# Kernel optimization log

Measured on AMD Instinct MI355X. Metric: run time of the kernel, lower is better.

Reference implementation:

```python
import jax, jax.numpy as jnp
import numpy as np

GNO_RADIUS = 0.1
SCALES = (1.0, 2.0)


def _rescale(x):
    # rescale coords per batch/dim to [-1, 1] (matches repo's rescale())
    mn = x.min(axis=1, keepdims=True)
    mx = x.max(axis=1, keepdims=True)
    return 2.0 * (x - mn) / (mx - mn + 1e-12) - 1.0


def setup_inputs() -> dict:
    key = jax.random.key(0)
    ks = jax.random.split(key, 6)
    B, N, M, Din, C, D, H = 2, 1024, 1024, 16, 32, 2, 32
    pndata = jax.random.normal(ks[0], (B, N, Din), dtype=jnp.float32)
    x_coord = jax.random.uniform(ks[1], (B, N, D), dtype=jnp.float32)
    # latent queries: regular 32x32 grid in [-1,1]^2 (regional node positions)
    g = jnp.linspace(-1.0, 1.0, 32, dtype=jnp.float32)
    latent_queries = jnp.stack(jnp.meshgrid(g, g, indexing='ij'), axis=-1).reshape(M, D)
    # lifting ChannelMLP (1 layer == pointwise linear)
    W_lift = jax.random.normal(ks[2], (Din, C), dtype=jnp.float32) / np.sqrt(Din)
    b_lift = jnp.zeros((C,), dtype=jnp.float32)
    # IntegralTransform kernel MLP: [2*D -> H -> C], gelu between layers
    W1 = jax.random.normal(ks[3], (2 * D, H), dtype=jnp.float32) / np.sqrt(2 * D)
    b1 = jnp.zeros((H,), dtype=jnp.float32)
    W2 = jax.random.normal(ks[4], (H, C), dtype=jnp.float32) / np.sqrt(H)
    b2 = jnp.zeros((C,), dtype=jnp.float32)
    return dict(pndata=pndata, x_coord=x_coord, latent_queries=latent_queries,
                W_lift=W_lift, b_lift=b_lift, W1=W1, b1=b1, W2=W2, b2=b2)


def reference(pndata, x_coord, latent_queries, W_lift, b_lift, W1, b1, W2, b2):
    # pndata: [B,N,Din], x_coord: [B,N,D], latent_queries: [M,D]
    x = _rescale(x_coord)                           # [B,N,D]
    f = pndata @ W_lift + b_lift                    # lifting -> [B,N,C]
    q = latent_queries                              # [M,D]
    B, N, D = x.shape
    M = q.shape[0]
    # squared distances query->point: [B,M,N]
    d2 = jnp.sum((q[None, :, None, :] - x[:, None, :, :]) ** 2, axis=-1)
    # kernel MLP input: concat(y_j, x_i) per (query i, point j): [B,M,N,2D]
    feat = jnp.concatenate([
        jnp.broadcast_to(x[:, None, :, :], (B, M, N, D)),
        jnp.broadcast_to(q[None, :, None, :], (B, M, N, D)),
    ], axis=-1)
    k = jax.nn.gelu(feat @ W1 + b1) @ W2 + b2       # [B,M,N,C]
    kv = k * f[:, None, :, :]                       # 'linear' transform: k(x,y) * f(y)
    out = jnp.zeros((B, M, kv.shape[-1]), dtype=kv.dtype)
    for s in SCALES:                                # small fixed scale set
        mask = (d2 <= (GNO_RADIUS * s) ** 2).astype(kv.dtype)   # radius-ball neighbors
        cnt = jnp.maximum(mask.sum(axis=-1), 1.0)               # [B,M]
        agg = jnp.einsum('bmn,bmnc->bmc', mask, kv) / cnt[..., None]  # mean reduce
        out = out + agg                              # sum over scales
    return out
```

## Files before the change

kernel.cpp:

```cpp
#include <hip/hip_runtime.h>

#define BB 2
#define NN 1024
#define MM 1024
#define DIN 16
#define CC 32
#define HH 32

__device__ __forceinline__ float gelu_tanh(float v) {
    float v3 = v * v * v;
    float u = 0.7978845608028654f * (v + 0.044715f * v3);
    float e = __expf(2.0f * u);
    float t = 1.0f - 2.0f / (e + 1.0f);
    return 0.5f * v * (1.0f + t);
}

__global__ __launch_bounds__(256) void gno_fused(
    const float* __restrict__ pndata, const float* __restrict__ x_coord,
    const float* __restrict__ latq,
    const float* __restrict__ W_lift, const float* __restrict__ b_lift,
    const float* __restrict__ W1, const float* __restrict__ b1,
    const float* __restrict__ W2, const float* __restrict__ b2,
    float* __restrict__ out)
{
    const int bid = blockIdx.x;
    const int b = bid >> 10;
    const int i = bid & 1023;
    const int t = threadIdx.x;
    const int lane = t & 63;
    const int wave = t >> 6;
    const int g = t >> 5;
    const int c = t & 31;

    __shared__ float2 nbr_xy[NN];
    __shared__ unsigned nbr_meta[NN];
    __shared__ __align__(16) float hbuf[8 * HH];
    __shared__ float accs[8 * CC];
    __shared__ float redf[4 * 4];
    __shared__ int kcnt[4];
    __shared__ int k1cnt[4];

    const float w1a = W1[c];
    const float w1b = W1[HH + c];
    const float w1c = W1[2 * HH + c];
    const float w1d = W1[3 * HH + c];
    const float b1v = b1[c];
    const float b2v = b2[c];
    const float blv = b_lift[c];
    float wl[DIN];
    #pragma unroll
    for (int k = 0; k < DIN; ++k) wl[k] = W_lift[k * CC + c];
    float w2c[HH];
    #pragma unroll
    for (int h = 0; h < HH; ++h) w2c[h] = W2[h * CC + c];

    const float q0 = latq[2 * i];
    const float q1 = latq[2 * i + 1];

    const float2* xcb = (const float2*)x_coord + b * NN;
    float2 xyc[4];
    float mn0 = 1e30f, mx0 = -1e30f, mn1 = 1e30f, mx1 = -1e30f;
    #pragma unroll
    for (int kk = 0; kk < 4; ++kk) {
        xyc[kk] = xcb[wave * 256 + kk * 64 + lane];
        mn0 = fminf(mn0, xyc[kk].x); mx0 = fmaxf(mx0, xyc[kk].x);
        mn1 = fminf(mn1, xyc[kk].y); mx1 = fmaxf(mx1, xyc[kk].y);
    }
    #pragma unroll
    for (int off = 32; off > 0; off >>= 1) {
        mn0 = fminf(mn0, __shfl_down(mn0, off));
        mx0 = fmaxf(mx0, __shfl_down(mx0, off));
        mn1 = fminf(mn1, __shfl_down(mn1, off));
        mx1 = fmaxf(mx1, __shfl_down(mx1, off));
    }
    if (lane == 0) {
        redf[wave * 4 + 0] = mn0; redf[wave * 4 + 1] = mx0;
        redf[wave * 4 + 2] = mn1; redf[wave * 4 + 3] = mx1;
    }
    __syncthreads();
    const float Amn0 = fminf(fminf(redf[0], redf[4]),  fminf(redf[8],  redf[12]));
    const float Amx0 = fmaxf(fmaxf(redf[1], redf[5]),  fmaxf(redf[9],  redf[13]));
    const float Amn1 = fminf(fminf(redf[2], redf[6]),  fminf(redf[10], redf[14]));
    const float Amx1 = fmaxf(fmaxf(redf[3], redf[7]),  fmaxf(redf[11], redf[15]));
    const float den0 = __fadd_rn(__fsub_rn(Amx0, Amn0), 1e-12f);
    const float den1 = __fadd_rn(__fsub_rn(Amx1, Amn1), 1e-12f);

    const float t1 = 0.01f;
    const float t2 = 0.04f;

    const unsigned long long lmask = (1ull << lane) - 1ull;
    int kw = 0, k1w = 0;
    #pragma unroll
    for (int kk = 0; kk < 4; ++kk) {
        const int j = wave * 256 + kk * 64 + lane;
        float r0 = __fsub_rn(__fdiv_rn(__fmul_rn(2.0f, __fsub_rn(xyc[kk].x, Amn0)), den0), 1.0f);
        float r1 = __fsub_rn(__fdiv_rn(__fmul_rn(2.0f, __fsub_rn(xyc[kk].y, Amn1)), den1), 1.0f);
        float dx = __fsub_rn(q0, r0);
        float dy = __fsub_rn(q1, r1);
        float d2 = __fadd_rn(__fmul_rn(dx, dx), __fmul_rn(dy, dy));
        bool h2 = d2 <= t2;
        bool h1 = d2 <= t1;
        unsigned long long m2 = __ballot(h2);
        unsigned long long m1 = __ballot(h1);
        if (h2) {
            int idx = wave * 256 + kw + __popcll(m2 & lmask);
            nbr_meta[idx] = (unsigned)j | (h1 ? 1024u : 0u);
            nbr_xy[idx] = make_float2(r0, r1);
        }
        kw += (int)__popcll(m2);
        k1w += (int)__popcll(m1);
    }
    if (lane == 0) { kcnt[wave] = kw; k1cnt[wave] = k1w; }
    __syncthreads();

    const int Ks0 = kcnt[0], Ks1 = kcnt[1], Ks2 = kcnt[2], Ks3 = kcnt[3];
    const int K2 = Ks0 + Ks1 + Ks2 + Ks3;
    const int c1 = k1cnt[0] + k1cnt[1] + k1cnt[2] + k1cnt[3];
    const float inv1 = 1.0f / fmaxf((float)c1, 1.0f);
    const float inv2 = 1.0f / fmaxf((float)K2, 1.0f);
    const float ci = fmaf(q1, w1d, fmaf(q0, w1c, b1v));

    float acc = 0.0f;
    #pragma unroll
    for (int seg = 0; seg < 4; ++seg) {
        const int Ks = (seg == 0) ? Ks0 : (seg == 1) ? Ks1 : (seg == 2) ? Ks2 : Ks3;
        const int base = seg * 256;
        const int nt = (Ks + 7) >> 3;
        for (int it = 0; it < nt; ++it) {
            const int ib = it * 8 + g;
            const bool active = ib < Ks;
            const int idx = base + (active ? ib : 0);
            const unsigned meta = nbr_meta[idx];
            const float2 xy = nbr_xy[idx];
            const int j = (int)(meta & 1023u);
            const float w = ((meta & 1024u) ? inv1 : 0.0f) + inv2;

            float pre = fmaf(xy.y, w1b, fmaf(xy.x, w1a, ci));
            hbuf[g * HH + c] = gelu_tanh(pre);

            float kc = b2v;
            const float4* hb4 = (const float4*)&hbuf[g * HH];
            #pragma unroll
            for (int hh = 0; hh < 8; ++hh) {
                float4 hv = hb4[hh];
                kc = fmaf(hv.x, w2c[4 * hh + 0], kc);
                kc = fmaf(hv.y, w2c[4 * hh + 1], kc);
                kc = fmaf(hv.z, w2c[4 * hh + 2], kc);
                kc = fmaf(hv.w, w2c[4 * hh + 3], kc);
            }

            const float4* pd4 = (const float4*)&pndata[(b * NN + j) * DIN];
            float fv = blv;
            #pragma unroll
            for (int k4 = 0; k4 < 4; ++k4) {
                float4 p = pd4[k4];
                fv = fmaf(p.x, wl[4 * k4 + 0], fv);
                fv = fmaf(p.y, wl[4 * k4 + 1], fv);
                fv = fmaf(p.z, wl[4 * k4 + 2], fv);
                fv = fmaf(p.w, wl[4 * k4 + 3], fv);
            }

            if (active) acc = fmaf(w, kc * fv, acc);
        }
    }
    accs[g * CC + c] = acc;
    __syncthreads();
    if (t < CC) {
        float s = 0.0f;
        #pragma unroll
        for (int g2 = 0; g2 < 8; ++g2) s += accs[g2 * CC + t];
        out[(b * MM + i) * CC + t] = s;
    }
}

extern "C" void kernel_launch(void* const* d_in, const int* in_sizes, int n_in,
                              void* d_out, int out_size, void* d_ws, size_t ws_size,
                              hipStream_t stream) {
    const float* pndata = (const float*)d_in[0];
    const float* x_coord = (const float*)d_in[1];
    const float* latq = (const float*)d_in[2];
    const float* W_lift = (const float*)d_in[3];
    const float* b_lift = (const float*)d_in[4];
    const float* W1 = (const float*)d_in[5];
    const float* b1 = (const float*)d_in[6];
    const float* W2 = (const float*)d_in[7];
    const float* b2 = (const float*)d_in[8];
    float* out = (float*)d_out;

    gno_fused<<<BB * MM, 256, 0, stream>>>(pndata, x_coord, latq,
                                           W_lift, b_lift, W1, b1, W2, b2, out);
}
```

Baseline: 20.01 us.

## Replace LDS hidden buffer with shuffles, hoist pndata loads, split FMA chains

The hidden-layer exchange now goes through 32-wide warp shuffles instead of writes and reads to the hbuf shared array. The pndata gather is issued before the GELU so its latency overlaps compute, and the FMA reductions are split into independent partial chains for more ILP. It also swaps the GELU division for a hardware reciprocal and loads the query as a float2. Shuffles on AMD are ds_bpermute or DPP operations, so the shared-memory savings may be small, and the reciprocal slightly changes rounding.

```diff
diff --git a/kernel.cpp b/kernel.cpp
--- a/kernel.cpp
+++ b/kernel.cpp
@@ -11,7 +11,7 @@
     float v3 = v * v * v;
     float u = 0.7978845608028654f * (v + 0.044715f * v3);
     float e = __expf(2.0f * u);
-    float t = 1.0f - 2.0f / (e + 1.0f);
+    float t = 1.0f - 2.0f * __builtin_amdgcn_rcpf(e + 1.0f);
     return 0.5f * v * (1.0f + t);
 }
 
@@ -34,7 +34,6 @@
 
     __shared__ float2 nbr_xy[NN];
     __shared__ unsigned nbr_meta[NN];
-    __shared__ __align__(16) float hbuf[8 * HH];
     __shared__ float accs[8 * CC];
     __shared__ float redf[4 * 4];
     __shared__ int kcnt[4];
@@ -54,8 +53,8 @@
     #pragma unroll
     for (int h = 0; h < HH; ++h) w2c[h] = W2[h * CC + c];
 
-    const float q0 = latq[2 * i];
-    const float q1 = latq[2 * i + 1];
+    const float2 qv = ((const float2*)latq)[i];
+    const float q0 = qv.x, q1 = qv.y;
 
     const float2* xcb = (const float2*)x_coord + b * NN;
     float2 xyc[4];
@@ -135,30 +134,32 @@
             const int j = (int)(meta & 1023u);
             const float w = ((meta & 1024u) ? inv1 : 0.0f) + inv2;
 
+            const float4* pd4 = (const float4*)&pndata[(b * NN + j) * DIN];
+            float4 pA = pd4[0], pB = pd4[1], pC = pd4[2], pD = pd4[3];
+
             float pre = fmaf(xy.y, w1b, fmaf(xy.x, w1a, ci));
-            hbuf[g * HH + c] = gelu_tanh(pre);
+            float myh = gelu_tanh(pre);
 
-            float kc = b2v;
-            const float4* hb4 = (const float4*)&hbuf[g * HH];
+            float p0 = b2v, p1 = 0.0f, p2 = 0.0f, p3 = 0.0f;
             #pragma unroll
-            for (int hh = 0; hh < 8; ++hh) {
-                float4 hv = hb4[hh];
-                kc = fmaf(hv.x, w2c[4 * hh + 0], kc);
-                kc = fmaf(hv.y, w2c[4 * hh + 1], kc);
-                kc = fmaf(hv.z, w2c[4 * hh + 2], kc);
-                kc = fmaf(hv.w, w2c[4 * hh + 3], kc);
+            for (int h = 0; h < 8; ++h) {
+                p0 = fmaf(__shfl(myh, h,      32), w2c[h],      p0);
+                p1 = fmaf(__shfl(myh, h + 8,  32), w2c[h + 8],  p1);
+                p2 = fmaf(__shfl(myh, h + 16, 32), w2c[h + 16], p2);
+                p3 = fmaf(__shfl(myh, h + 24, 32), w2c[h + 24], p3);
             }
+            float kc = (p0 + p1) + (p2 + p3);
 
-            const float4* pd4 = (const float4*)&pndata[(b * NN + j) * DIN];
-            float fv = blv;
-            #pragma unroll
-            for (int k4 = 0; k4 < 4; ++k4) {
-                float4 p = pd4[k4];
-                fv = fmaf(p.x, wl[4 * k4 + 0], fv);
-                fv = fmaf(p.y, wl[4 * k4 + 1], fv);
-                fv = fmaf(p.z, wl[4 * k4 + 2], fv);
-                fv = fmaf(p.w, wl[4 * k4 + 3], fv);
-            }
+            float f0 = blv, f1 = 0.0f;
+            f0 = fmaf(pA.x, wl[0],  f0); f1 = fmaf(pA.y, wl[1],  f1);
+            f0 = fmaf(pA.z, wl[2],  f0); f1 = fmaf(pA.w, wl[3],  f1);
+            f0 = fmaf(pB.x, wl[4],  f0); f1 = fmaf(pB.y, wl[5],  f1);
+            f0 = fmaf(pB.z, wl[6],  f0); f1 = fmaf(pB.w, wl[7],  f1);
+            f0 = fmaf(pC.x, wl[8],  f0); f1 = fmaf(pC.y, wl[9],  f1);
+            f0 = fmaf(pC.z, wl[10], f0); f1 = fmaf(pC.w, wl[11], f1);
+            f0 = fmaf(pD.x, wl[12], f0); f1 = fmaf(pD.y, wl[13], f1);
+            f0 = fmaf(pD.z, wl[14], f0); f1 = fmaf(pD.w, wl[15], f1);
+            float fv = f0 + f1;
 
             if (active) acc = fmaf(w, kc * fv, acc);
         }
```

Result: slower. 29.62 us (+48.0%).
